# Kernel optimization log

Hardware: AMD Instinct MI355X
Metric: run time of the kernel (lower is better)

The kernel has to match this reference:

```python
import jax, jax.numpy as jnp
import numpy as np

B, L, S, H = 2, 256, 384, 768
Tc, Dc = 16, 50
WV, WD = 20000, 100
CV = 128
NEG = -1e30


def _lstm_scan(x, Wih, Whh, bih, bhh):
    # x: [N, T, D] -> hs: [N, T, Hc]; torch LSTM gate order i,f,g,o
    N = x.shape[0]
    Hc = Whh.shape[1]
    h0 = jnp.zeros((N, Hc), x.dtype)

    def step(carry, xt):
        h, c = carry
        g = xt @ Wih.T + h @ Whh.T + bih + bhh  # [N, 4Hc]
        i, f, gg, o = jnp.split(g, 4, axis=-1)
        i = jax.nn.sigmoid(i)
        f = jax.nn.sigmoid(f)
        gg = jnp.tanh(gg)
        o = jax.nn.sigmoid(o)
        c = f * c + i * gg
        h = o * jnp.tanh(c)
        return (h, c), h

    _, hs = jax.lax.scan(step, (h0, h0), jnp.swapaxes(x, 0, 1))
    return jnp.swapaxes(hs, 0, 1)


def setup_inputs() -> dict:
    key = jax.random.key(0)
    ks = jax.random.split(key, 10)
    bert_emb = jax.random.normal(ks[0], (B, S, H), jnp.float32)
    pieces2word = jax.random.randint(ks[1], (B, L, S), 0, 2, jnp.int32)
    word_ids = jax.random.randint(ks[2], (B, L), 0, WV, jnp.int32)
    char_count = jax.random.randint(ks[3], (B, L), 1, Tc + 1, jnp.int32)
    char_ids = jax.random.randint(ks[4], (B, L, Tc), 0, CV, jnp.int32)
    # mask consistent with ragged char lengths (first char_count positions valid)
    token_masks_char = (jnp.arange(Tc)[None, None, :] < char_count[..., None]).astype(jnp.int32)
    word_table = jax.random.normal(ks[5], (WV, WD), jnp.float32) * 0.02
    char_table = jax.random.normal(ks[6], (CV, Dc), jnp.float32) * 0.02
    sc = 1.0 / np.sqrt(Dc)

    def lstm_w(k):
        a, b, c, d = jax.random.split(k, 4)
        return (jax.random.uniform(a, (4 * Dc, Dc), jnp.float32, -sc, sc),
                jax.random.uniform(b, (4 * Dc, Dc), jnp.float32, -sc, sc),
                jax.random.uniform(c, (4 * Dc,), jnp.float32, -sc, sc),
                jax.random.uniform(d, (4 * Dc,), jnp.float32, -sc, sc))

    Wih_f, Whh_f, bih_f, bhh_f = lstm_w(ks[7])
    Wih_b, Whh_b, bih_b, bhh_b = lstm_w(ks[8])
    return dict(bert_emb=bert_emb, pieces2word=pieces2word, word_ids=word_ids,
                char_count=char_count, char_ids=char_ids, token_masks_char=token_masks_char,
                word_table=word_table, char_table=char_table,
                Wih_f=Wih_f, Whh_f=Whh_f, bih_f=bih_f, bhh_f=bhh_f,
                Wih_b=Wih_b, Whh_b=Whh_b, bih_b=bih_b, bhh_b=bhh_b)


def reference(bert_emb, pieces2word, word_ids, char_count, char_ids, token_masks_char,
              word_table, char_table, Wih_f, Whh_f, bih_f, bhh_f, Wih_b, Whh_b, bih_b, bhh_b):
    # --- piece2word max pool (expand + masked_fill(min) + max over pieces) ---
    minv = jnp.min(bert_emb)
    # [B, L, S, H] intermediate, as in the original expand
    masked = jnp.where(pieces2word[..., None] != 0, bert_emb[:, None, :, :], minv)
    word_reps = jnp.max(masked, axis=2)  # [B, L, H]
    # dropouts are identity in eval mode

    # --- word embedding lookup ---
    word_embed = word_table[word_ids]  # [B, L, WD]

    # --- char bi-LSTM with packed-sequence semantics ---
    lens = jnp.maximum(char_count.reshape(-1), 1)  # char_count[char_count==0]=1
    x = char_table[char_ids.reshape(B * L, Tc)]  # [N, Tc, Dc]
    h_fwd = _lstm_scan(x, Wih_f, Whh_f, bih_f, bhh_f)
    # reverse each sequence within its valid length for the backward direction
    t = jnp.arange(Tc)[None, :]
    idx = jnp.where(t < lens[:, None], lens[:, None] - 1 - t, t)  # [N, Tc]
    x_rev = jnp.take_along_axis(x, idx[..., None], axis=1)
    h_bwd = _lstm_scan(x_rev, Wih_b, Whh_b, bih_b, bhh_b)
    h_bwd = jnp.take_along_axis(h_bwd, idx[..., None], axis=1)  # back to original order
    h = jnp.concatenate([h_fwd, h_bwd], axis=-1)  # [N, Tc, 2*Dc]
    valid = (t < lens[:, None])[..., None]
    h = jnp.where(valid, h, 0.0)  # pad_packed_sequence zero-pads beyond length
    h = h.reshape(B, L, Tc, 2 * Dc)

    # --- combine(..., 'max'): masked max over ragged char groups ---
    m = jnp.where(token_masks_char[..., None] == 0, NEG, 0.0)
    sup = jnp.max(m + h, axis=2)  # [B, L, 2*Dc]
    sup = jnp.where(sup == NEG, 0.0, sup)

    return jnp.concatenate([word_reps, word_embed, sup], axis=-1)  # [B, L, H+WD+2*Dc]
```

## Files before the change

kernel.cpp:

```cpp
#include <hip/hip_runtime.h>
#include <float.h>

#define Bb 2
#define Ll 256
#define Ss 384
#define Hh 768
#define Tc 16
#define Dc 50
#define WD 100
#define CV 128
#define NG 200
#define OUTC 968


__device__ inline float tanh_fast(float x) {
    float e = __expf(2.f * x);
    return 1.f - 2.f / (e + 1.f);
}
__device__ inline float sigmoid_fast(float x) {
    return 1.f / (1.f + __expf(-x));
}


__global__ __launch_bounds__(256) void prep_kernel(
        const float* __restrict__ bert, const float* __restrict__ char_table,
        const float* __restrict__ Wih_f, const float* __restrict__ bih_f, const float* __restrict__ bhh_f,
        const float* __restrict__ Wih_b, const float* __restrict__ bih_b, const float* __restrict__ bhh_b,
        const int* __restrict__ word_ids, const float* __restrict__ word_table,
        float* __restrict__ minp, float* __restrict__ xpt, float* __restrict__ out) {
    int blk = blockIdx.x, tid = threadIdx.x;
    if (blk < 128) {
        const int n4 = (Bb * Ss * Hh) / 4;
        const float4* b4 = (const float4*)bert;
        float m = FLT_MAX;
        for (int i = blk * 256 + tid; i < n4; i += 128 * 256) {
            float4 v = b4[i];
            m = fminf(m, fminf(fminf(v.x, v.y), fminf(v.z, v.w)));
        }
        #pragma unroll
        for (int off = 32; off; off >>= 1) m = fminf(m, __shfl_down(m, off, 64));
        __shared__ float red[4];
        if ((tid & 63) == 0) red[tid >> 6] = m;
        __syncthreads();
        if (tid == 0) minp[blk] = fminf(fminf(red[0], red[1]), fminf(red[2], red[3]));
    } else if (blk < 192) {
        int idx = blk - 128;
        int dir = idx >> 5, c0 = (idx & 31) * 4;
        const float* Wih = dir ? Wih_b : Wih_f;
        const float* bih = dir ? bih_b : bih_f;
        const float* bhh = dir ? bhh_b : bhh_f;
        __shared__ float ct[4][Dc];
        if (tid < 4 * Dc) ((float*)ct)[tid] = char_table[c0 * Dc + tid];
        __syncthreads();
        if (tid < NG) {
            float w[Dc];
            #pragma unroll
            for (int j = 0; j < Dc; j++) w[j] = Wih[tid * Dc + j];
            float bias = bih[tid] + bhh[tid];
            #pragma unroll
            for (int cid = 0; cid < 4; cid++) {
                float a = bias;
                #pragma unroll
                for (int j = 0; j < Dc; j++) a += w[j] * ct[cid][j];
                xpt[(dir * CV + c0 + cid) * NG + tid] = a;
            }
        }
    } else {
        for (int i = (blk - 192) * 256 + tid; i < Bb * Ll * WD; i += 64 * 256) {
            int bl = i / WD, d = i - bl * WD;
            out[(size_t)bl * OUTC + Hh + d] = word_table[(size_t)word_ids[bl] * WD + d];
        }
    }
}


__global__ __launch_bounds__(512) void word_kernel(
        const float* __restrict__ bert, const int* __restrict__ p2w,
        const float* __restrict__ minp, float* __restrict__ out) {
    __shared__ float sacc[8][8][256];
    __shared__ float sminv;
    int tid = threadIdx.x;
    int wv = tid >> 6, lane = tid & 63;

    if (tid < 64) {
        float m = fminf(minp[tid], minp[tid + 64]);
        #pragma unroll
        for (int off = 32; off; off >>= 1) m = fminf(m, __shfl_down(m, off, 64));
        if (tid == 0) sminv = m;
    }

    int idx = blockIdx.x;
    int hc = idx % 3;
    int lt = (idx / 3) & 31;
    int b  = idx / 96;
    int l0 = lt * 8;
    int s0 = wv * 48;

    const int* pm = p2w + ((size_t)(b * Ll + l0)) * Ss + s0;
    unsigned mlo[8], mhi[8];
    #pragma unroll
    for (int r = 0; r < 8; r++) {
        unsigned long long bal = __ballot(lane < 48 ? (pm[r * Ss + lane] != 0) : false);
        mlo[r] = __builtin_amdgcn_readfirstlane((unsigned)bal);
        mhi[r] = __builtin_amdgcn_readfirstlane((unsigned)(bal >> 32));
    }

    const float4* bb4 = (const float4*)(bert + (size_t)b * Ss * Hh) + hc * 64 + lane;
    float4 acc[8];
    #pragma unroll
    for (int r = 0; r < 8; r++) { acc[r].x = acc[r].y = acc[r].z = acc[r].w = -FLT_MAX; }

    for (int jo = 0; jo < 48; jo += 8) {
        float4 v[8];
        #pragma unroll
        for (int k = 0; k < 8; k++) v[k] = bb4[(size_t)(s0 + jo + k) * 192];
        #pragma unroll
        for (int k = 0; k < 8; k++) {
            int j = jo + k;
            #pragma unroll
            for (int r = 0; r < 8; r++) {
                unsigned bit = (j < 32 ? mlo[r] >> j : mhi[r] >> (j - 32)) & 1u;
                if (bit) {
                    acc[r].x = fmaxf(acc[r].x, v[k].x);
                    acc[r].y = fmaxf(acc[r].y, v[k].y);
                    acc[r].z = fmaxf(acc[r].z, v[k].z);
                    acc[r].w = fmaxf(acc[r].w, v[k].w);
                }
            }
        }
    }
    #pragma unroll
    for (int r = 0; r < 8; r++)
        *(float4*)&sacc[wv][r][lane * 4] = acc[r];
    __syncthreads();

    float mv = sminv;
    #pragma unroll
    for (int e = tid; e < 8 * 256; e += 512) {
        int r = e >> 8, cx = e & 255;
        float m = sacc[0][r][cx];
        #pragma unroll
        for (int k = 1; k < 8; k++) m = fmaxf(m, sacc[k][r][cx]);
        if (m == -FLT_MAX) m = mv;
        out[((size_t)(b * Ll + l0 + r)) * OUTC + hc * 256 + cx] = m;
    }
}


__global__ __launch_bounds__(64, 1) void lstm_kernel(
        const int* __restrict__ char_ids, const int* __restrict__ char_count,
        const float* __restrict__ Whh_f, const float* __restrict__ Whh_b,
        const float* __restrict__ xpt, float* __restrict__ out) {
    int blk = blockIdx.x;
    int n = blk >> 1, dir = blk & 1;
    int lane = threadIdx.x;
    const float* Whh = dir ? Whh_b : Whh_f;
    __shared__ __align__(16) float hs[52];

    int len = char_count[n];
    if (len < 1) len = 1;

    int cidv = 0;
    if (lane < Tc) {
        int st = dir ? (lane < len ? len - 1 - lane : lane) : lane;
        cidv = char_ids[n * Tc + st];
    }

    float w[4][52];
    if (lane < Dc) {
        #pragma unroll
        for (int q = 0; q < 4; q++) {
            const float2* wr = (const float2*)(Whh + (q * Dc + lane) * Dc);
            #pragma unroll
            for (int m = 0; m < 25; m++) {
                float2 t = wr[m];
                w[q][2 * m] = t.x; w[q][2 * m + 1] = t.y;
            }
        }
    }
    #pragma unroll
    for (int q = 0; q < 4; q++) { w[q][50] = 0.f; w[q][51] = 0.f; }

    if (lane < 52) hs[lane] = 0.f;
    __syncthreads();

    int cid0 = __shfl(cidv, 0);
    const float* xr = xpt + (size_t)(dir * CV + cid0) * NG;
    float xp[4];
    #pragma unroll
    for (int q = 0; q < 4; q++) xp[q] = (lane < Dc) ? xr[q * Dc + lane] : 0.f;

    float c = 0.f, h = 0.f, maxv = -FLT_MAX;
    for (int t = 0; t < Tc; t++) {
        int tn = (t + 1 < Tc) ? t + 1 : t;
        int cidn = __shfl(cidv, tn);
        const float* xrn = xpt + (size_t)(dir * CV + cidn) * NG;
        float xpn[4];
        #pragma unroll
        for (int q = 0; q < 4; q++) xpn[q] = (lane < Dc) ? xrn[q * Dc + lane] : 0.f;

        float g0 = xp[0], g1 = xp[1], g2 = xp[2], g3 = xp[3];
        #pragma unroll
        for (int m = 0; m < 13; m++) {
            float4 hv = *(const float4*)&hs[4 * m];
            g0 += hv.x * w[0][4*m] + hv.y * w[0][4*m+1] + hv.z * w[0][4*m+2] + hv.w * w[0][4*m+3];
            g1 += hv.x * w[1][4*m] + hv.y * w[1][4*m+1] + hv.z * w[1][4*m+2] + hv.w * w[1][4*m+3];
            g2 += hv.x * w[2][4*m] + hv.y * w[2][4*m+1] + hv.z * w[2][4*m+2] + hv.w * w[2][4*m+3];
            g3 += hv.x * w[3][4*m] + hv.y * w[3][4*m+1] + hv.z * w[3][4*m+2] + hv.w * w[3][4*m+3];
        }
        if (lane < Dc) {
            float si = sigmoid_fast(g0);
            float sf = sigmoid_fast(g1);
            float tg = tanh_fast(g2);
            float so = sigmoid_fast(g3);
            c = sf * c + si * tg;
            h = so * tanh_fast(c);
            if (t < len) maxv = fmaxf(maxv, h);
        }
        __syncthreads();
        if (lane < Dc) hs[lane] = h;
        __syncthreads();
        #pragma unroll
        for (int q = 0; q < 4; q++) xp[q] = xpn[q];
    }
    if (lane < Dc)
        out[(size_t)n * OUTC + (Hh + WD) + dir * Dc + lane] = maxv;
}

extern "C" void kernel_launch(void* const* d_in, const int* in_sizes, int n_in,
                              void* d_out, int out_size, void* d_ws, size_t ws_size,
                              hipStream_t stream) {
    const float* bert       = (const float*)d_in[0];
    const int*   p2w        = (const int*)d_in[1];
    const int*   word_ids   = (const int*)d_in[2];
    const int*   char_count = (const int*)d_in[3];
    const int*   char_ids   = (const int*)d_in[4];
    const float* word_table = (const float*)d_in[6];
    const float* char_table = (const float*)d_in[7];
    const float* Wih_f = (const float*)d_in[8];
    const float* Whh_f = (const float*)d_in[9];
    const float* bih_f = (const float*)d_in[10];
    const float* bhh_f = (const float*)d_in[11];
    const float* Wih_b = (const float*)d_in[12];
    const float* Whh_b = (const float*)d_in[13];
    const float* bih_b = (const float*)d_in[14];
    const float* bhh_b = (const float*)d_in[15];
    float* out = (float*)d_out;

    float* minp = (float*)d_ws;
    float* xpt  = minp + 128;

    prep_kernel<<<256, 256, 0, stream>>>(
        bert, char_table, Wih_f, bih_f, bhh_f, Wih_b, bih_b, bhh_b,
        word_ids, word_table, minp, xpt, out);
    word_kernel<<<192, 512, 0, stream>>>(bert, p2w, minp, out);
    lstm_kernel<<<1024, 64, 0, stream>>>(
        char_ids, char_count, Whh_f, Whh_b, xpt, out);
}
```

Before: 127.9 us.

## Fuse word max-pool and char LSTM into one kernel with packed LSTM waves

Merges the word max-pooling kernel and the char BiLSTM kernel into a single launch. The first 384 blocks run the pooling with a finer hidden split (float2, 6 chunks instead of 3). The remaining 128 blocks each pack 8 independent LSTM sequences as separate waves with per-wave shared state. This is meant to remove a launch and let the two independent stages overlap on the GPU. Packing waves into 512-thread blocks also makes the per-step __syncthreads span all 8 waves, which couples independent sequences, and the large per-lane register arrays may limit occupancy.

```diff
diff --git a/kernel.cpp b/kernel.cpp
--- a/kernel.cpp
+++ b/kernel.cpp
@@ -74,157 +74,155 @@
 }
 
 
-__global__ __launch_bounds__(512) void word_kernel(
+__global__ __launch_bounds__(512, 2) void fused_kernel(
         const float* __restrict__ bert, const int* __restrict__ p2w,
-        const float* __restrict__ minp, float* __restrict__ out) {
-    __shared__ float sacc[8][8][256];
-    __shared__ float sminv;
-    int tid = threadIdx.x;
-    int wv = tid >> 6, lane = tid & 63;
-
-    if (tid < 64) {
-        float m = fminf(minp[tid], minp[tid + 64]);
-        #pragma unroll
-        for (int off = 32; off; off >>= 1) m = fminf(m, __shfl_down(m, off, 64));
-        if (tid == 0) sminv = m;
-    }
-
-    int idx = blockIdx.x;
-    int hc = idx % 3;
-    int lt = (idx / 3) & 31;
-    int b  = idx / 96;
-    int l0 = lt * 8;
-    int s0 = wv * 48;
-
-    const int* pm = p2w + ((size_t)(b * Ll + l0)) * Ss + s0;
-    unsigned mlo[8], mhi[8];
-    #pragma unroll
-    for (int r = 0; r < 8; r++) {
-        unsigned long long bal = __ballot(lane < 48 ? (pm[r * Ss + lane] != 0) : false);
-        mlo[r] = __builtin_amdgcn_readfirstlane((unsigned)bal);
-        mhi[r] = __builtin_amdgcn_readfirstlane((unsigned)(bal >> 32));
-    }
-
-    const float4* bb4 = (const float4*)(bert + (size_t)b * Ss * Hh) + hc * 64 + lane;
-    float4 acc[8];
-    #pragma unroll
-    for (int r = 0; r < 8; r++) { acc[r].x = acc[r].y = acc[r].z = acc[r].w = -FLT_MAX; }
-
-    for (int jo = 0; jo < 48; jo += 8) {
-        float4 v[8];
-        #pragma unroll
-        for (int k = 0; k < 8; k++) v[k] = bb4[(size_t)(s0 + jo + k) * 192];
-        #pragma unroll
-        for (int k = 0; k < 8; k++) {
-            int j = jo + k;
-            #pragma unroll
-            for (int r = 0; r < 8; r++) {
-                unsigned bit = (j < 32 ? mlo[r] >> j : mhi[r] >> (j - 32)) & 1u;
-                if (bit) {
-                    acc[r].x = fmaxf(acc[r].x, v[k].x);
-                    acc[r].y = fmaxf(acc[r].y, v[k].y);
-                    acc[r].z = fmaxf(acc[r].z, v[k].z);
-                    acc[r].w = fmaxf(acc[r].w, v[k].w);
-                }
-            }
-        }
-    }
-    #pragma unroll
-    for (int r = 0; r < 8; r++)
-        *(float4*)&sacc[wv][r][lane * 4] = acc[r];
-    __syncthreads();
-
-    float mv = sminv;
-    #pragma unroll
-    for (int e = tid; e < 8 * 256; e += 512) {
-        int r = e >> 8, cx = e & 255;
-        float m = sacc[0][r][cx];
-        #pragma unroll
-        for (int k = 1; k < 8; k++) m = fmaxf(m, sacc[k][r][cx]);
-        if (m == -FLT_MAX) m = mv;
-        out[((size_t)(b * Ll + l0 + r)) * OUTC + hc * 256 + cx] = m;
-    }
-}
-
-
-__global__ __launch_bounds__(64, 1) void lstm_kernel(
+        const float* __restrict__ minp,
         const int* __restrict__ char_ids, const int* __restrict__ char_count,
         const float* __restrict__ Whh_f, const float* __restrict__ Whh_b,
         const float* __restrict__ xpt, float* __restrict__ out) {
-    int blk = blockIdx.x;
-    int n = blk >> 1, dir = blk & 1;
-    int lane = threadIdx.x;
-    const float* Whh = dir ? Whh_b : Whh_f;
-    __shared__ __align__(16) float hs[52];
-
-    int len = char_count[n];
-    if (len < 1) len = 1;
-
-    int cidv = 0;
-    if (lane < Tc) {
-        int st = dir ? (lane < len ? len - 1 - lane : lane) : lane;
-        cidv = char_ids[n * Tc + st];
+    __shared__ __align__(16) char smem[32896];
+    int blk = blockIdx.x, tid = threadIdx.x;
+    int wv = tid >> 6, lane = tid & 63;
+
+    if (blk < 384) {
+        float (*sacc)[8][128] = (float (*)[8][128])smem;
+        float* sminv = (float*)(smem + 32768);
+
+        if (tid < 64) {
+            float m = fminf(minp[tid], minp[tid + 64]);
+            #pragma unroll
+            for (int off = 32; off; off >>= 1) m = fminf(m, __shfl_down(m, off, 64));
+            if (tid == 0) *sminv = m;
+        }
+        int hc = blk % 6;
+        int lt = (blk / 6) & 31;
+        int b  = blk / 192;
+        int l0 = lt * 8;
+        int s0 = wv * 48;
+
+        const int* pm = p2w + ((size_t)(b * Ll + l0)) * Ss + s0;
+        unsigned mlo[8], mhi[8];
+        #pragma unroll
+        for (int r = 0; r < 8; r++) {
+            unsigned long long bal = __ballot(lane < 48 ? (pm[r * Ss + lane] != 0) : false);
+            mlo[r] = __builtin_amdgcn_readfirstlane((unsigned)bal);
+            mhi[r] = __builtin_amdgcn_readfirstlane((unsigned)(bal >> 32));
+        }
+
+        const float2* bb2 = (const float2*)(bert + (size_t)b * Ss * Hh) + hc * 64 + lane;
+        float2 acc[8];
+        #pragma unroll
+        for (int r = 0; r < 8; r++) { acc[r].x = -FLT_MAX; acc[r].y = -FLT_MAX; }
+
+        for (int jo = 0; jo < 48; jo += 8) {
+            float2 v[8];
+            #pragma unroll
+            for (int k = 0; k < 8; k++) v[k] = bb2[(size_t)(s0 + jo + k) * 384];
+            #pragma unroll
+            for (int k = 0; k < 8; k++) {
+                int j = jo + k;
+                #pragma unroll
+                for (int r = 0; r < 8; r++) {
+                    unsigned bit = (j < 32 ? mlo[r] >> j : mhi[r] >> (j - 32)) & 1u;
+                    if (bit) {
+                        acc[r].x = fmaxf(acc[r].x, v[k].x);
+                        acc[r].y = fmaxf(acc[r].y, v[k].y);
+                    }
+                }
+            }
+        }
+        #pragma unroll
+        for (int r = 0; r < 8; r++)
+            *(float2*)&sacc[wv][r][lane * 2] = acc[r];
+        __syncthreads();
+
+        float mv = *sminv;
+        #pragma unroll
+        for (int e = tid; e < 8 * 128; e += 512) {
+            int r = e >> 7, cx = e & 127;
+            float m = sacc[0][r][cx];
+            #pragma unroll
+            for (int k = 1; k < 8; k++) m = fmaxf(m, sacc[k][r][cx]);
+            if (m == -FLT_MAX) m = mv;
+            out[((size_t)(b * Ll + l0 + r)) * OUTC + hc * 128 + cx] = m;
+        }
+    } else {
+        float (*hs)[52] = (float (*)[52])smem;
+        float* hsw = hs[wv];
+
+        int wid = (blk - 384) * 8 + wv;
+        int n = wid >> 1, dir = wid & 1;
+        const float* Whh = dir ? Whh_b : Whh_f;
+
+        int len = char_count[n];
+        if (len < 1) len = 1;
+
+        int cidv = 0;
+        if (lane < Tc) {
+            int st = dir ? (lane < len ? len - 1 - lane : lane) : lane;
+            cidv = char_ids[n * Tc + st];
+        }
+
+        float w[4][52];
+        if (lane < Dc) {
+            #pragma unroll
+            for (int q = 0; q < 4; q++) {
+                const float2* wr = (const float2*)(Whh + (q * Dc + lane) * Dc);
+                #pragma unroll
+                for (int m = 0; m < 25; m++) {
+                    float2 t = wr[m];
+                    w[q][2 * m] = t.x; w[q][2 * m + 1] = t.y;
+                }
+            }
+        }
+        #pragma unroll
+        for (int q = 0; q < 4; q++) { w[q][50] = 0.f; w[q][51] = 0.f; }
+
+        if (lane < 52) hsw[lane] = 0.f;
+        __syncthreads();
+
+        int cid0 = __shfl(cidv, 0);
+        const float* xr = xpt + (size_t)(dir * CV + cid0) * NG;
+        float xp[4];
+        #pragma unroll
+        for (int q = 0; q < 4; q++) xp[q] = (lane < Dc) ? xr[q * Dc + lane] : 0.f;
+
+        float c = 0.f, h = 0.f, maxv = -FLT_MAX;
+        for (int t = 0; t < Tc; t++) {
+            int tn = (t + 1 < Tc) ? t + 1 : t;
+            int cidn = __shfl(cidv, tn);
+            const float* xrn = xpt + (size_t)(dir * CV + cidn) * NG;
+            float xpn[4];
+            #pragma unroll
+            for (int q = 0; q < 4; q++) xpn[q] = (lane < Dc) ? xrn[q * Dc + lane] : 0.f;
+
+            float g0 = xp[0], g1 = xp[1], g2 = xp[2], g3 = xp[3];
+            #pragma unroll
+            for (int m = 0; m < 13; m++) {
+                float4 hv = *(const float4*)&hsw[4 * m];
+                g0 += hv.x * w[0][4*m] + hv.y * w[0][4*m+1] + hv.z * w[0][4*m+2] + hv.w * w[0][4*m+3];
+                g1 += hv.x * w[1][4*m] + hv.y * w[1][4*m+1] + hv.z * w[1][4*m+2] + hv.w * w[1][4*m+3];
+                g2 += hv.x * w[2][4*m] + hv.y * w[2][4*m+1] + hv.z * w[2][4*m+2] + hv.w * w[2][4*m+3];
+                g3 += hv.x * w[3][4*m] + hv.y * w[3][4*m+1] + hv.z * w[3][4*m+2] + hv.w * w[3][4*m+3];
+            }
+            if (lane < Dc) {
+                float si = sigmoid_fast(g0);
+                float sf = sigmoid_fast(g1);
+                float tg = tanh_fast(g2);
+                float so = sigmoid_fast(g3);
+                c = sf * c + si * tg;
+                h = so * tanh_fast(c);
+                if (t < len) maxv = fmaxf(maxv, h);
+            }
+            __syncthreads();
+            if (lane < Dc) hsw[lane] = h;
+            __syncthreads();
+            #pragma unroll
+            for (int q = 0; q < 4; q++) xp[q] = xpn[q];
+        }
+        if (lane < Dc)
+            out[(size_t)n * OUTC + (Hh + WD) + dir * Dc + lane] = maxv;
     }
-
-    float w[4][52];
-    if (lane < Dc) {
-        #pragma unroll
-        for (int q = 0; q < 4; q++) {
-            const float2* wr = (const float2*)(Whh + (q * Dc + lane) * Dc);
-            #pragma unroll
-            for (int m = 0; m < 25; m++) {
-                float2 t = wr[m];
-                w[q][2 * m] = t.x; w[q][2 * m + 1] = t.y;
-            }
-        }
-    }
-    #pragma unroll
-    for (int q = 0; q < 4; q++) { w[q][50] = 0.f; w[q][51] = 0.f; }
-
-    if (lane < 52) hs[lane] = 0.f;
-    __syncthreads();
-
-    int cid0 = __shfl(cidv, 0);
-    const float* xr = xpt + (size_t)(dir * CV + cid0) * NG;
-    float xp[4];
-    #pragma unroll
-    for (int q = 0; q < 4; q++) xp[q] = (lane < Dc) ? xr[q * Dc + lane] : 0.f;
-
-    float c = 0.f, h = 0.f, maxv = -FLT_MAX;
-    for (int t = 0; t < Tc; t++) {
-        int tn = (t + 1 < Tc) ? t + 1 : t;
-        int cidn = __shfl(cidv, tn);
-        const float* xrn = xpt + (size_t)(dir * CV + cidn) * NG;
-        float xpn[4];
-        #pragma unroll
-        for (int q = 0; q < 4; q++) xpn[q] = (lane < Dc) ? xrn[q * Dc + lane] : 0.f;
-
-        float g0 = xp[0], g1 = xp[1], g2 = xp[2], g3 = xp[3];
-        #pragma unroll
-        for (int m = 0; m < 13; m++) {
-            float4 hv = *(const float4*)&hs[4 * m];
-            g0 += hv.x * w[0][4*m] + hv.y * w[0][4*m+1] + hv.z * w[0][4*m+2] + hv.w * w[0][4*m+3];
-            g1 += hv.x * w[1][4*m] + hv.y * w[1][4*m+1] + hv.z * w[1][4*m+2] + hv.w * w[1][4*m+3];
-            g2 += hv.x * w[2][4*m] + hv.y * w[2][4*m+1] + hv.z * w[2][4*m+2] + hv.w * w[2][4*m+3];
-            g3 += hv.x * w[3][4*m] + hv.y * w[3][4*m+1] + hv.z * w[3][4*m+2] + hv.w * w[3][4*m+3];
-        }
-        if (lane < Dc) {
-            float si = sigmoid_fast(g0);
-            float sf = sigmoid_fast(g1);
-            float tg = tanh_fast(g2);
-            float so = sigmoid_fast(g3);
-            c = sf * c + si * tg;
-            h = so * tanh_fast(c);
-            if (t < len) maxv = fmaxf(maxv, h);
-        }
-        __syncthreads();
-        if (lane < Dc) hs[lane] = h;
-        __syncthreads();
-        #pragma unroll
-        for (int q = 0; q < 4; q++) xp[q] = xpn[q];
-    }
-    if (lane < Dc)
-        out[(size_t)n * OUTC + (Hh + WD) + dir * Dc + lane] = maxv;
 }
 
 extern "C" void kernel_launch(void* const* d_in, const int* in_sizes, int n_in,
@@ -253,7 +251,6 @@
     prep_kernel<<<256, 256, 0, stream>>>(
         bert, char_table, Wih_f, bih_f, bhh_f, Wih_b, bih_b, bhh_b,
         word_ids, word_table, minp, xpt, out);
-    word_kernel<<<192, 512, 0, stream>>>(bert, p2w, minp, out);
-    lstm_kernel<<<1024, 64, 0, stream>>>(
-        char_ids, char_count, Whh_f, Whh_b, xpt, out);
-}
+    fused_kernel<<<512, 512, 0, stream>>>(
+        bert, p2w, minp, char_ids, char_count, Whh_f, Whh_b, xpt, out);
+}
```

Measured after the change: 175.4 us. 37.1% more time.
